# Optimization experiments

Measured on AMD Instinct MI355X. Metric: run time of the kernel, lower is better.

Reference implementation:

```python
import jax, jax.numpy as jnp
import numpy as np

COST_CLASS = 2.0
COST_BBOX = 5.0
COST_GIOU = 2.0
ALPHA = 0.25
GAMMA = 2.0
EPS = 1e-8


def box_cxcywh_to_xyxy(b):
    cx, cy, w, h = b[..., 0], b[..., 1], b[..., 2], b[..., 3]
    return jnp.stack([cx - 0.5 * w, cy - 0.5 * h, cx + 0.5 * w, cy + 0.5 * h], axis=-1)


def pairwise_giou(boxes1, boxes2):
    # boxes1: [N,4] xyxy, boxes2: [T,4] xyxy -> [N,T]
    area1 = (boxes1[:, 2] - boxes1[:, 0]) * (boxes1[:, 3] - boxes1[:, 1])
    area2 = (boxes2[:, 2] - boxes2[:, 0]) * (boxes2[:, 3] - boxes2[:, 1])
    lt = jnp.maximum(boxes1[:, None, :2], boxes2[None, :, :2])   # [N,T,2]
    rb = jnp.minimum(boxes1[:, None, 2:], boxes2[None, :, 2:])
    wh = jnp.clip(rb - lt, 0.0)
    inter = wh[..., 0] * wh[..., 1]
    union = area1[:, None] + area2[None, :] - inter
    iou = inter / union
    # smallest enclosing box
    lt_e = jnp.minimum(boxes1[:, None, :2], boxes2[None, :, :2])
    rb_e = jnp.maximum(boxes1[:, None, 2:], boxes2[None, :, 2:])
    wh_e = jnp.clip(rb_e - lt_e, 0.0)
    area_e = wh_e[..., 0] * wh_e[..., 1]
    return iou - (area_e - union) / area_e


def setup_inputs() -> dict:
    key = jax.random.key(0)
    k1, k2, k3, k4 = jax.random.split(key, 4)
    bs, nq, nc, nt = 16, 900, 91, 1600
    return {
        "pred_logits": jax.random.normal(k1, (bs, nq, nc), dtype=jnp.float32),
        "pred_boxes": jax.random.uniform(k2, (bs, nq, 4), dtype=jnp.float32),
        "tgt_boxes": jax.random.uniform(k3, (nt, 4), dtype=jnp.float32),
        "tgt_ids": jax.random.randint(k4, (nt,), 0, nc, dtype=jnp.int64),
    }


def reference(pred_logits, pred_boxes, tgt_boxes, tgt_ids):
    bs, nq, _ = pred_logits.shape
    out_prob = jax.nn.sigmoid(pred_logits.reshape(bs * nq, -1).astype(jnp.float32))
    out_bbox = pred_boxes.reshape(bs * nq, 4).astype(jnp.float32)
    tgt_bbox = tgt_boxes.astype(jnp.float32)

    # focal classification cost, gathered at target class columns: [N,T]
    p = out_prob[:, tgt_ids]
    neg_cost = (1.0 - ALPHA) * (p ** GAMMA) * (-jnp.log(1.0 - p + EPS))
    pos_cost = ALPHA * ((1.0 - p) ** GAMMA) * (-jnp.log(p + EPS))
    cost_class = pos_cost - neg_cost

    # L1 box cost (cdist p=1): [N,T]
    cost_bbox = jnp.abs(out_bbox[:, None, :] - tgt_bbox[None, :, :]).sum(-1)

    # GIoU cost: [N,T]
    cost_giou = -pairwise_giou(box_cxcywh_to_xyxy(out_bbox), box_cxcywh_to_xyxy(tgt_bbox))

    C = COST_BBOX * cost_bbox + COST_CLASS * cost_class + COST_GIOU * cost_giou
    return C.reshape(bs, nq, -1)
```

## Files before the change

### kernel.cpp

```cpp
#include <hip/hip_runtime.h>


#define BLOCK 256
#define QPB 8
#define NC 91
#define NT 1600
#define TSLOTS ((NT + BLOCK - 1) / BLOCK)

__global__ __launch_bounds__(BLOCK, 4) void matcher_kernel(
    const float* __restrict__ logits,
    const float* __restrict__ pboxes,
    const float* __restrict__ tboxes,
    const int*   __restrict__ tids,
    float*       __restrict__ out)
{
    __shared__ float s_cc[QPB * NC];
    const int tid = threadIdx.x;
    const int q0  = blockIdx.x * QPB;

    for (int i = tid; i < QPB * NC; i += BLOCK) {
        float x   = logits[(size_t)q0 * NC + i];
        float p   = 1.0f / (1.0f + __expf(-x));
        float omp = 1.0f - p;
        float pos = 0.25f * omp * omp * (-__logf(p   + 1e-8f));
        float neg = 0.75f * p   * p   * (-__logf(omp + 1e-8f));
        s_cc[i] = 2.0f * (pos - neg);
    }

    float4 tb[TSLOTS], xy[TSLOTS];
    int    ida[TSLOTS];
    #pragma unroll
    for (int k = 0; k < TSLOTS; ++k) {
        int t = tid + k * BLOCK;
        if (t < NT) {
            float4 b = ((const float4*)tboxes)[t];
            tb[k] = b;
            xy[k] = make_float4(fmaf(-0.5f, b.z, b.x), fmaf(-0.5f, b.w, b.y),
                                fmaf( 0.5f, b.z, b.x), fmaf( 0.5f, b.w, b.y));
            ida[k] = tids[t];
        }
    }
    __syncthreads();

    #pragma unroll 1
    for (int q = 0; q < QPB; ++q) {
        const int    qg = q0 + q;
        const float4 qb = ((const float4*)pboxes)[qg];
        const float qx0 = fmaf(-0.5f, qb.z, qb.x), qy0 = fmaf(-0.5f, qb.w, qb.y);
        const float qx1 = fmaf( 0.5f, qb.z, qb.x), qy1 = fmaf( 0.5f, qb.w, qb.y);
        const float qarea = qb.z * qb.w;
        const float* cc   = s_cc + q * NC;
        float* outq = out + (size_t)qg * NT;

        #pragma unroll
        for (int k = 0; k < TSLOTS; ++k) {
            int t = tid + k * BLOCK;
            if (t < NT) {
                float4 b = tb[k], p = xy[k];

                float l1 = fabsf(qb.x - b.x) + fabsf(qb.y - b.y)
                         + fabsf(qb.z - b.z) + fabsf(qb.w - b.w);

                float tarea = b.z * b.w;
                float iw = fminf(qx1, p.z) - fmaxf(qx0, p.x);
                float ih = fminf(qy1, p.w) - fmaxf(qy0, p.y);
                float inter = fmaxf(iw, 0.0f) * fmaxf(ih, 0.0f);
                float uni   = qarea + tarea - inter;
                float iou   = inter * __builtin_amdgcn_rcpf(uni);
                float ew = fmaxf(qx1, p.z) - fminf(qx0, p.x);
                float eh = fmaxf(qy1, p.w) - fminf(qy0, p.y);
                float earea = ew * eh;
                float giou  = iou - (earea - uni) * __builtin_amdgcn_rcpf(earea);

                outq[t] = fmaf(5.0f, l1, cc[ida[k]]) - 2.0f * giou;
            }
        }
    }
}

extern "C" void kernel_launch(void* const* d_in, const int* in_sizes, int n_in,
                              void* d_out, int out_size, void* d_ws, size_t ws_size,
                              hipStream_t stream) {
    const float* logits = (const float*)d_in[0];
    const float* pboxes = (const float*)d_in[1];
    const float* tboxes = (const float*)d_in[2];
    const int*   tids   = (const int*)d_in[3];

    const int nqall = in_sizes[1] / 4;
    float* out = (float*)d_out;

    matcher_kernel<<<nqall / QPB, BLOCK, 0, stream>>>(logits, pboxes, tboxes,
                                                      tids, out);
}
```

Measured before the change: 121.4 us.

## Restructure matcher to emit float4 output stores with LDS-staged target data

Each thread now computes four adjacent target columns and writes them with a single 16-byte store. A flattened (query, column-group) index covers 16 queries per block. Target corners and class ids are precomputed into LDS in SoA float4 form, query corners are staged in LDS, and the L1 term is derived from the xyxy corner differences. The aim is to cut store instruction count and per-element ALU work on this output-write-bound kernel. The cost is more LDS traffic per element, a per-slot integer division, and half as many blocks.

```diff
diff --git a/kernel.cpp b/kernel.cpp
--- a/kernel.cpp
+++ b/kernel.cpp
@@ -2,10 +2,11 @@
 
 
 #define BLOCK 256
-#define QPB 8
-#define NC 91
-#define NT 1600
-#define TSLOTS ((NT + BLOCK - 1) / BLOCK)
+#define QPB   16
+#define NC    91
+#define NT    1600
+#define NCOL  (NT / 4)
+#define SLOTS (QPB * NCOL / BLOCK)
 
 __global__ __launch_bounds__(BLOCK, 4) void matcher_kernel(
     const float* __restrict__ logits,
@@ -14,7 +15,11 @@
     const int*   __restrict__ tids,
     float*       __restrict__ out)
 {
-    __shared__ float s_cc[QPB * NC];
+    __shared__ float4 s_x0[NCOL], s_y0[NCOL], s_x1[NCOL], s_y1[NCOL];
+    __shared__ int4   s_id[NCOL];
+    __shared__ float  s_cc[QPB * NC];
+    __shared__ float  s_q[QPB][8];
+
     const int tid = threadIdx.x;
     const int q0  = blockIdx.x * QPB;
 
@@ -27,54 +32,72 @@
         s_cc[i] = 2.0f * (pos - neg);
     }
 
-    float4 tb[TSLOTS], xy[TSLOTS];
-    int    ida[TSLOTS];
-    #pragma unroll
-    for (int k = 0; k < TSLOTS; ++k) {
-        int t = tid + k * BLOCK;
-        if (t < NT) {
-            float4 b = ((const float4*)tboxes)[t];
-            tb[k] = b;
-            xy[k] = make_float4(fmaf(-0.5f, b.z, b.x), fmaf(-0.5f, b.w, b.y),
-                                fmaf( 0.5f, b.z, b.x), fmaf( 0.5f, b.w, b.y));
-            ida[k] = tids[t];
-        }
+    for (int t = tid; t < NT; t += BLOCK) {
+        float4 b = ((const float4*)tboxes)[t];
+        ((float*)s_x0)[t] = fmaf(-0.5f, b.z, b.x);
+        ((float*)s_y0)[t] = fmaf(-0.5f, b.w, b.y);
+        ((float*)s_x1)[t] = fmaf( 0.5f, b.z, b.x);
+        ((float*)s_y1)[t] = fmaf( 0.5f, b.w, b.y);
+        ((int*)  s_id)[t] = tids[t];
+    }
+
+    if (tid < QPB) {
+        float4 b = ((const float4*)pboxes)[q0 + tid];
+        s_q[tid][0] = fmaf(-0.5f, b.z, b.x);
+        s_q[tid][1] = fmaf(-0.5f, b.w, b.y);
+        s_q[tid][2] = fmaf( 0.5f, b.z, b.x);
+        s_q[tid][3] = fmaf( 0.5f, b.w, b.y);
+        s_q[tid][4] = b.z * b.w;
     }
     __syncthreads();
 
     #pragma unroll 1
-    for (int q = 0; q < QPB; ++q) {
-        const int    qg = q0 + q;
-        const float4 qb = ((const float4*)pboxes)[qg];
-        const float qx0 = fmaf(-0.5f, qb.z, qb.x), qy0 = fmaf(-0.5f, qb.w, qb.y);
-        const float qx1 = fmaf( 0.5f, qb.z, qb.x), qy1 = fmaf( 0.5f, qb.w, qb.y);
-        const float qarea = qb.z * qb.w;
-        const float* cc   = s_cc + q * NC;
-        float* outq = out + (size_t)qg * NT;
+    for (int s = 0; s < SLOTS; ++s) {
+        const unsigned idx = (unsigned)(s * BLOCK + tid);
+        const unsigned q   = idx / 400u;
+        const unsigned c   = idx - q * 400u;
+
+        const float qx0 = s_q[q][0], qy0 = s_q[q][1];
+        const float qx1 = s_q[q][2], qy1 = s_q[q][3];
+        const float qarea = s_q[q][4];
+        const float* cc = s_cc + q * NC;
+
+        const float4 X0 = s_x0[c], Y0 = s_y0[c], X1 = s_x1[c], Y1 = s_y1[c];
+        const int4   ID = s_id[c];
+
+        const float x0a[4] = {X0.x, X0.y, X0.z, X0.w};
+        const float y0a[4] = {Y0.x, Y0.y, Y0.z, Y0.w};
+        const float x1a[4] = {X1.x, X1.y, X1.z, X1.w};
+        const float y1a[4] = {Y1.x, Y1.y, Y1.z, Y1.w};
+        const int   ida[4] = {ID.x, ID.y, ID.z, ID.w};
+        float r[4];
 
         #pragma unroll
-        for (int k = 0; k < TSLOTS; ++k) {
-            int t = tid + k * BLOCK;
-            if (t < NT) {
-                float4 b = tb[k], p = xy[k];
+        for (int j = 0; j < 4; ++j) {
+            const float x0 = x0a[j], y0 = y0a[j], x1 = x1a[j], y1 = y1a[j];
 
-                float l1 = fabsf(qb.x - b.x) + fabsf(qb.y - b.y)
-                         + fabsf(qb.z - b.z) + fabsf(qb.w - b.w);
+            const float dx0 = x0 - qx0, dx1 = x1 - qx1;
+            const float dy0 = y0 - qy0, dy1 = y1 - qy1;
+            const float e = fabsf(dx0 + dx1) + fabsf(dy0 + dy1);
+            const float f = fabsf(dx1 - dx0) + fabsf(dy1 - dy0);
 
-                float tarea = b.z * b.w;
-                float iw = fminf(qx1, p.z) - fmaxf(qx0, p.x);
-                float ih = fminf(qy1, p.w) - fmaxf(qy0, p.y);
-                float inter = fmaxf(iw, 0.0f) * fmaxf(ih, 0.0f);
-                float uni   = qarea + tarea - inter;
-                float iou   = inter * __builtin_amdgcn_rcpf(uni);
-                float ew = fmaxf(qx1, p.z) - fminf(qx0, p.x);
-                float eh = fmaxf(qy1, p.w) - fminf(qy0, p.y);
-                float earea = ew * eh;
-                float giou  = iou - (earea - uni) * __builtin_amdgcn_rcpf(earea);
+            const float iw = fminf(qx1, x1) - fmaxf(qx0, x0);
+            const float ih = fminf(qy1, y1) - fmaxf(qy0, y0);
+            const float inter = fmaxf(iw, 0.0f) * fmaxf(ih, 0.0f);
+            const float tarea = (x1 - x0) * (y1 - y0);
+            const float uni   = qarea + tarea - inter;
+            const float iou   = inter * __builtin_amdgcn_rcpf(uni);
 
-                outq[t] = fmaf(5.0f, l1, cc[ida[k]]) - 2.0f * giou;
-            }
+            const float ew = fmaxf(qx1, x1) - fminf(qx0, x0);
+            const float eh = fmaxf(qy1, y1) - fminf(qy0, y0);
+            const float earea = ew * eh;
+            const float g = iou - (earea - uni) * __builtin_amdgcn_rcpf(earea);
+
+            r[j] = fmaf(2.5f, e, fmaf(5.0f, f, fmaf(-2.0f, g, cc[ida[j]])));
         }
+
+        ((float4*)(out + (size_t)(q0 + q) * NT + c * 4u))[0] =
+            make_float4(r[0], r[1], r[2], r[3]);
     }
 }
 
```

After: 126.2 us. 4.0% more time.
